# Performance work log

Hardware: AMD Instinct MI355X
Metric: run time of the kernel (lower is better)

The kernel has to match this reference:

```python
import jax, jax.numpy as jnp
import numpy as np

NEG_INF = -1e30  # stand-in for -inf that is safe under fp16/bf16


def setup_inputs() -> dict:
    key = jax.random.key(0)
    k1, k2, k3, k4, k5 = jax.random.split(key, 5)
    B, NC, H, Wd = 32, 256, 64, 64
    MW, E = 32, 768
    images = jax.random.normal(k1, (B, NC, H, Wd), dtype=jnp.float32)
    words = jax.random.normal(k2, (B, MW, E), dtype=jnp.float32)
    # mask: True where word is ignored; ensure at least one word is attended per row
    mask = jax.random.randint(k3, (B, MW), 0, 2).astype(bool)
    mask = mask.at[:, 0].set(False)
    W = jax.random.normal(k4, (NC, E), dtype=jnp.float32) * (1.0 / np.sqrt(E))
    b = jax.random.normal(k5, (NC,), dtype=jnp.float32) * 0.01
    return {"images": images, "words": words, "mask": mask, "W": W, "b": b}


def reference(images, words, mask, W, b):
    B, NC, H, Wd = images.shape
    _, MW, E = words.shape
    # 1x1 conv over words == linear projection emb_dim -> nc_in
    # words_p: [B, nc_in, max_words]
    words_p = jnp.einsum('bme,ce->bcm', words, W) + b[None, :, None]
    # images flattened to pixels: [B, h*w, nc_in]
    imgs = images.reshape(B, NC, H * Wd).transpose(0, 2, 1)
    # attention scores: [B, h*w, max_words], scaled by 1/sqrt(nc_in)
    attn = jnp.einsum('bpc,bcm->bpm', imgs, words_p) * (1.0 / np.sqrt(NC))
    attn = jnp.where(mask[:, None, :], NEG_INF, attn)
    attn = jax.nn.softmax(attn, axis=-1)
    # weighted word sum per pixel: [B, nc_in, h*w]
    weighted = jnp.einsum('bcm,bpm->bcp', words_p, attn)
    weighted_words = weighted.reshape(B, NC, H, Wd)
    attn_out = attn.transpose(0, 2, 1).reshape(B, MW, H, Wd)
    return weighted_words, attn_out
```

## Files before the change

### kernel.cpp

```cpp
#include <hip/hip_runtime.h>
#include <math.h>

#define B_   32
#define NC_  256
#define HW_  4096
#define MW_  32
#define E_   768
#define NEG_BIG -3.0e38f

#define PART_OFF   0
#define WP_OFF     2097152
#define WT_OFF     2359296
#define WORDST_OFF 2555904
#define MASK_OFF   3342336

__global__ __launch_bounds__(256) void prep_kernel(
    const float* __restrict__ W, const float* __restrict__ words,
    const void* __restrict__ mask_raw,
    float* __restrict__ WT, float* __restrict__ wordsT,
    int* __restrict__ maskn) {
  const int tid = threadIdx.x;
  const int tx = tid & 31, ty = tid >> 5;
  if (blockIdx.x < 192) {
    __shared__ float t[32][33];
    const int tc = blockIdx.x / 24, te = blockIdx.x % 24;
    const int c0 = tc * 32, e0 = te * 32;
#pragma unroll
    for (int k = 0; k < 4; ++k) {
      const int r = ty + 8 * k;
      t[r][tx] = W[(c0 + r) * E_ + e0 + tx];
    }
    __syncthreads();
#pragma unroll
    for (int k = 0; k < 4; ++k) {
      const int r = ty + 8 * k;
      WT[(e0 + r) * NC_ + c0 + tx] = t[tx][r];
    }
  } else if (blockIdx.x < 960) {
    __shared__ float t[32][33];
    const int idx = blockIdx.x - 192;
    const int b = idx / 24, te = idx % 24;
    const int e0 = te * 32;
    const float* wsrc = words + (size_t)b * MW_ * E_;
    float* wdst = wordsT + (size_t)b * E_ * MW_;
#pragma unroll
    for (int k = 0; k < 4; ++k) {
      const int m = ty + 8 * k;
      t[m][tx] = wsrc[m * E_ + e0 + tx];
    }
    __syncthreads();
#pragma unroll
    for (int k = 0; k < 4; ++k) {
      const int e = ty + 8 * k;
      wdst[(e0 + e) * MW_ + tx] = t[tx][e];
    }
  } else {
    __shared__ int is_word;
    if (tid == 0) is_word = 1;
    __syncthreads();
    const int* mi = (const int*)mask_raw;
    const int v = mi[tid];
    if (v != 0 && v != 1 && v != 0x3F800000) is_word = 0;
    __syncthreads();
    if (is_word) {
#pragma unroll
      for (int j = 0; j < 4; ++j) { const int i = j * 256 + tid; maskn[i] = (mi[i] != 0); }
    } else {
      const unsigned char* mb = (const unsigned char*)mask_raw;
#pragma unroll
      for (int j = 0; j < 4; ++j) { const int i = j * 256 + tid; maskn[i] = (mb[i] != 0); }
    }
  }
}

__global__ __launch_bounds__(256) void stage1_partial(
    const float* __restrict__ wordsT, const float* __restrict__ WT,
    float* __restrict__ part) {
  const int c = threadIdx.x;
  const int b = blockIdx.x >> 3;
  const int chunk = blockIdx.x & 7;
  const int e0 = chunk * 96;
  const float* wt = wordsT + (size_t)b * E_ * MW_;
  float acc[32];
#pragma unroll
  for (int m = 0; m < 32; ++m) acc[m] = 0.f;
#pragma unroll 2
  for (int e = e0; e < e0 + 96; ++e) {
    const float wv = WT[(size_t)e * NC_ + c];
    const float* wr = wt + e * MW_;
#pragma unroll
    for (int m = 0; m < 32; ++m) acc[m] = fmaf(wv, wr[m], acc[m]);
  }
  float* pp = part + ((size_t)chunk * 32 + b) * 32 * 256;
#pragma unroll
  for (int m = 0; m < 32; ++m) pp[m * 256 + c] = acc[m];
}

__global__ __launch_bounds__(256) void stage1_reduce(
    const float* __restrict__ part, const float* __restrict__ bias,
    float* __restrict__ wp) {
  const int idx = blockIdx.x * 256 + threadIdx.x;
  const int c = idx & 255;
  const int m = (idx >> 8) & 31;
  const int b = idx >> 13;
  float s = bias[c];
#pragma unroll
  for (int k = 0; k < 8; ++k)
    s += part[(((size_t)k * 32 + b) * 32 + m) * 256 + c];
  wp[((size_t)b * 256 + c) * 32 + m] = s;
}

__global__ __launch_bounds__(256) void attention_fused(
    const float* __restrict__ images, const float* __restrict__ wp,
    const int* __restrict__ maskn, float* __restrict__ out_w,
    float* __restrict__ out_a) {
  __shared__ float lwp[NC_ * MW_];
  const int tid = threadIdx.x;
  const int b = blockIdx.x >> 4;
  const int p = ((blockIdx.x & 15) << 8) + tid;
  const float* img = images + (size_t)b * NC_ * HW_ + p;
  const float* wpb = wp + (size_t)b * NC_ * MW_;

  {
    const float4* src = (const float4*)wpb;
    float4* dst = (float4*)lwp;
#pragma unroll
    for (int k = 0; k < 8; ++k) dst[tid + (k << 8)] = src[tid + (k << 8)];
  }
  __syncthreads();

  float s[32];
#pragma unroll
  for (int m = 0; m < 32; ++m) s[m] = 0.f;

  float cur[16];
#pragma unroll
  for (int j = 0; j < 16; ++j)
    cur[j] = __builtin_nontemporal_load(img + ((size_t)j << 12));

#pragma unroll 1
  for (int c0 = 0; c0 < 256; c0 += 16) {
    float nxt[16];
    if (c0 + 16 < 256) {
#pragma unroll
      for (int j = 0; j < 16; ++j)
        nxt[j] = __builtin_nontemporal_load(img + ((size_t)(c0 + 16 + j) << 12));
    }
#pragma unroll
    for (int j = 0; j < 16; ++j) {
      const float* wrow = lwp + ((c0 + j) << 5);
#pragma unroll
      for (int m = 0; m < 32; ++m)
        s[m] = fmaf(cur[j], wrow[m], s[m]);
    }
#pragma unroll
    for (int j = 0; j < 16; ++j) cur[j] = nxt[j];
  }

  unsigned mbits = 0;
#pragma unroll
  for (int m = 0; m < 32; ++m)
    mbits |= (maskn[(b << 5) + m] != 0 ? 1u : 0u) << m;

  float mx = NEG_BIG;
#pragma unroll
  for (int m = 0; m < 32; ++m) {
    s[m] *= 0.0625f;
    if (!((mbits >> m) & 1u)) mx = fmaxf(mx, s[m]);
  }
  float sum = 0.f;
#pragma unroll
  for (int m = 0; m < 32; ++m) {
    const float ev = ((mbits >> m) & 1u) ? 0.f : __expf(s[m] - mx);
    s[m] = ev;
    sum += ev;
  }
  const float inv = 1.f / sum;
#pragma unroll
  for (int m = 0; m < 32; ++m) {
    const float a = s[m] * inv;
    s[m] = a;
    __builtin_nontemporal_store(a, out_a + ((size_t)(b * 32 + m) << 12) + p);
  }

#pragma unroll 1
  for (int c0 = 0; c0 < 256; c0 += 8) {
#pragma unroll
    for (int jc = 0; jc < 8; ++jc) {
      const int c = c0 + jc;
      const float* wrow = lwp + (c << 5);
      float o = 0.f;
#pragma unroll
      for (int m = 0; m < 32; ++m)
        o = fmaf(wrow[m], s[m], o);
      __builtin_nontemporal_store(o, out_w + ((size_t)(b * 256 + c) << 12) + p);
    }
  }
}

extern "C" void kernel_launch(void* const* d_in, const int* in_sizes, int n_in,
                              void* d_out, int out_size, void* d_ws, size_t ws_size,
                              hipStream_t stream) {
  const float* images = (const float*)d_in[0];
  const float* words  = (const float*)d_in[1];
  const void*  mask   = d_in[2];
  const float* W      = (const float*)d_in[3];
  const float* bias   = (const float*)d_in[4];

  float* ws     = (float*)d_ws;
  float* part   = ws + PART_OFF;
  float* wp     = ws + WP_OFF;
  float* WT     = ws + WT_OFF;
  float* wordsT = ws + WORDST_OFF;
  int*   maskn  = (int*)(ws + MASK_OFF);

  float* out_w = (float*)d_out;
  float* out_a = out_w + (size_t)B_ * NC_ * HW_;

  prep_kernel<<<961, 256, 0, stream>>>(W, words, mask, WT, wordsT, maskn);
  stage1_partial<<<256, 256, 0, stream>>>(wordsT, WT, part);
  stage1_reduce<<<1024, 256, 0, stream>>>(part, bias, wp);
  attention_fused<<<512, 256, 0, stream>>>(images, wp, maskn, out_w, out_a);
}
```

Measured before the change: 316.3 us.

## Process two pixels per thread in attention kernel with vectorized float2 I/O

Each thread of the fused attention kernel now handles two adjacent pixels, with 128-thread blocks. Image loads and both output stores use float2. Every LDS read of a projected-word weight now feeds two FMAs, halving shared-memory traffic per FLOP. The block-to-batch mapping is interleaved and the image prefetch is issued before the LDS fill. The cost is roughly double the register state (two 32-wide score arrays), with launch bounds set to 128 threads and at least one block per SM, so occupancy and latency hiding may drop.

```diff
diff --git a/kernel.cpp b/kernel.cpp
--- a/kernel.cpp
+++ b/kernel.cpp
@@ -7,6 +7,9 @@
 #define MW_  32
 #define E_   768
 #define NEG_BIG -3.0e38f
+
+typedef float vf2 __attribute__((ext_vector_type(2)));
+typedef float vf4 __attribute__((ext_vector_type(4)));
 
 #define PART_OFF   0
 #define WP_OFF     2097152
@@ -110,48 +113,50 @@
   wp[((size_t)b * 256 + c) * 32 + m] = s;
 }
 
-__global__ __launch_bounds__(256) void attention_fused(
+__global__ __launch_bounds__(128, 1) void attention_fused(
     const float* __restrict__ images, const float* __restrict__ wp,
     const int* __restrict__ maskn, float* __restrict__ out_w,
     float* __restrict__ out_a) {
   __shared__ float lwp[NC_ * MW_];
   const int tid = threadIdx.x;
-  const int b = blockIdx.x >> 4;
-  const int p = ((blockIdx.x & 15) << 8) + tid;
-  const float* img = images + (size_t)b * NC_ * HW_ + p;
-  const float* wpb = wp + (size_t)b * NC_ * MW_;
+  const int b = blockIdx.x & 31;
+  const int po = ((blockIdx.x >> 5) << 7) + tid;
+  const vf2* imgb = (const vf2*)(images + (size_t)b * NC_ * HW_);
+
+  vf2 cur[16];
+#pragma unroll
+  for (int j = 0; j < 16; ++j)
+    cur[j] = __builtin_nontemporal_load(&imgb[((size_t)j << 11) + po]);
 
   {
-    const float4* src = (const float4*)wpb;
-    float4* dst = (float4*)lwp;
-#pragma unroll
-    for (int k = 0; k < 8; ++k) dst[tid + (k << 8)] = src[tid + (k << 8)];
+    const vf4* src = (const vf4*)(wp + (size_t)b * NC_ * MW_);
+    vf4* dst = (vf4*)lwp;
+#pragma unroll
+    for (int k = 0; k < 16; ++k) dst[tid + (k << 7)] = src[tid + (k << 7)];
   }
   __syncthreads();
 
-  float s[32];
-#pragma unroll
-  for (int m = 0; m < 32; ++m) s[m] = 0.f;
-
-  float cur[16];
-#pragma unroll
-  for (int j = 0; j < 16; ++j)
-    cur[j] = __builtin_nontemporal_load(img + ((size_t)j << 12));
+  float s0[32], s1[32];
+#pragma unroll
+  for (int m = 0; m < 32; ++m) { s0[m] = 0.f; s1[m] = 0.f; }
 
 #pragma unroll 1
   for (int c0 = 0; c0 < 256; c0 += 16) {
-    float nxt[16];
+    vf2 nxt[16];
     if (c0 + 16 < 256) {
 #pragma unroll
       for (int j = 0; j < 16; ++j)
-        nxt[j] = __builtin_nontemporal_load(img + ((size_t)(c0 + 16 + j) << 12));
+        nxt[j] = __builtin_nontemporal_load(&imgb[((size_t)(c0 + 16 + j) << 11) + po]);
     }
 #pragma unroll
     for (int j = 0; j < 16; ++j) {
       const float* wrow = lwp + ((c0 + j) << 5);
-#pragma unroll
-      for (int m = 0; m < 32; ++m)
-        s[m] = fmaf(cur[j], wrow[m], s[m]);
+      const vf2 v = cur[j];
+#pragma unroll
+      for (int m = 0; m < 32; ++m) {
+        s0[m] = fmaf(v.x, wrow[m], s0[m]);
+        s1[m] = fmaf(v.y, wrow[m], s1[m]);
+      }
     }
 #pragma unroll
     for (int j = 0; j < 16; ++j) cur[j] = nxt[j];
@@ -162,38 +167,50 @@
   for (int m = 0; m < 32; ++m)
     mbits |= (maskn[(b << 5) + m] != 0 ? 1u : 0u) << m;
 
-  float mx = NEG_BIG;
+  float mx0 = NEG_BIG, mx1 = NEG_BIG;
 #pragma unroll
   for (int m = 0; m < 32; ++m) {
-    s[m] *= 0.0625f;
-    if (!((mbits >> m) & 1u)) mx = fmaxf(mx, s[m]);
-  }
-  float sum = 0.f;
+    s0[m] *= 0.0625f;
+    s1[m] *= 0.0625f;
+    if (!((mbits >> m) & 1u)) {
+      mx0 = fmaxf(mx0, s0[m]);
+      mx1 = fmaxf(mx1, s1[m]);
+    }
+  }
+  float sum0 = 0.f, sum1 = 0.f;
 #pragma unroll
   for (int m = 0; m < 32; ++m) {
-    const float ev = ((mbits >> m) & 1u) ? 0.f : __expf(s[m] - mx);
-    s[m] = ev;
-    sum += ev;
-  }
-  const float inv = 1.f / sum;
+    const bool msk = (mbits >> m) & 1u;
+    const float e0 = msk ? 0.f : __expf(s0[m] - mx0);
+    const float e1 = msk ? 0.f : __expf(s1[m] - mx1);
+    s0[m] = e0; s1[m] = e1;
+    sum0 += e0; sum1 += e1;
+  }
+  const float inv0 = 1.f / sum0, inv1 = 1.f / sum1;
+  vf2* oa = (vf2*)out_a;
 #pragma unroll
   for (int m = 0; m < 32; ++m) {
-    const float a = s[m] * inv;
-    s[m] = a;
-    __builtin_nontemporal_store(a, out_a + ((size_t)(b * 32 + m) << 12) + p);
-  }
-
+    s0[m] *= inv0;
+    s1[m] *= inv1;
+    vf2 a; a.x = s0[m]; a.y = s1[m];
+    __builtin_nontemporal_store(a, &oa[((size_t)((b << 5) + m) << 11) + po]);
+  }
+
+  vf2* ow = (vf2*)out_w;
 #pragma unroll 1
   for (int c0 = 0; c0 < 256; c0 += 8) {
 #pragma unroll
     for (int jc = 0; jc < 8; ++jc) {
       const int c = c0 + jc;
       const float* wrow = lwp + (c << 5);
-      float o = 0.f;
-#pragma unroll
-      for (int m = 0; m < 32; ++m)
-        o = fmaf(wrow[m], s[m], o);
-      __builtin_nontemporal_store(o, out_w + ((size_t)(b * 256 + c) << 12) + p);
+      float o0 = 0.f, o1 = 0.f;
+#pragma unroll
+      for (int m = 0; m < 32; ++m) {
+        o0 = fmaf(wrow[m], s0[m], o0);
+        o1 = fmaf(wrow[m], s1[m], o1);
+      }
+      vf2 o; o.x = o0; o.y = o1;
+      __builtin_nontemporal_store(o, &ow[((size_t)((b << 8) + c) << 11) + po]);
     }
   }
 }
@@ -220,5 +237,5 @@
   prep_kernel<<<961, 256, 0, stream>>>(W, words, mask, WT, wordsT, maskn);
   stage1_partial<<<256, 256, 0, stream>>>(wordsT, WT, part);
   stage1_reduce<<<1024, 256, 0, stream>>>(part, bias, wp);
-  attention_fused<<<512, 256, 0, stream>>>(images, wp, maskn, out_w, out_a);
-}
+  attention_fused<<<512, 128, 0, stream>>>(images, wp, maskn, out_w, out_a);
+}
```

Measured after the change: 308.3 us, median of 2. 2.5% less time.
